# Kernel tuning notes

Hardware: AMD Instinct MI355X
Metric: run time of the kernel (lower is better)

Reference implementation:

```python
import jax, jax.numpy as jnp
import numpy as np

N_NODES = 100000
N_EDGES = 1600000
D = 128
K = 3
LEAKY_ALPHA = 0.2  # tf.nn.leaky_relu default
L2_EPS = 1e-12     # tf.math.l2_normalize default


def spmm(row, col, val, x, n_nodes):
    # y[r] = sum_{e: row[e]==r} val[e] * x[col[e]]
    return jax.ops.segment_sum(val[:, None] * x[col], row, num_segments=n_nodes)


def setup_inputs() -> dict:
    key = jax.random.key(0)
    ks = jax.random.split(key, 8)
    embeddings = jax.random.normal(ks[0], (N_NODES, D), dtype=jnp.float32) * 0.1
    edge_row = jax.random.randint(ks[1], (N_EDGES,), 0, N_NODES, dtype=jnp.int32)
    edge_col = jax.random.randint(ks[2], (N_EDGES,), 0, N_NODES, dtype=jnp.int32)
    # normalized-laplacian-like positive weights
    edge_val = jax.random.uniform(ks[3], (N_EDGES,), dtype=jnp.float32) * 0.05
    W_gc = jax.random.normal(ks[4], (K, D, D), dtype=jnp.float32) * (1.0 / np.sqrt(D))
    b_gc = jax.random.normal(ks[5], (K, D), dtype=jnp.float32) * 0.01
    W_bi = jax.random.normal(ks[6], (K, D, D), dtype=jnp.float32) * (1.0 / np.sqrt(D))
    b_bi = jax.random.normal(ks[7], (K, D), dtype=jnp.float32) * 0.01
    return {"embeddings": embeddings, "edge_row": edge_row, "edge_col": edge_col,
            "edge_val": edge_val, "W_gc": W_gc, "b_gc": b_gc, "W_bi": W_bi, "b_bi": b_bi}


def reference(embeddings, edge_row, edge_col, edge_val, W_gc, b_gc, W_bi, b_bi):
    n = embeddings.shape[0]
    x = embeddings
    depth_embeddings = [x]
    for i in range(W_gc.shape[0]):
        Lx = spmm(edge_row, edge_col, edge_val, x, n)   # L @ x  (L has zero diag)
        prop = Lx + x                                    # S @ x, S = L with diag 1
        emb = prop @ W_gc[i] + b_gc[i][None, :]
        bi = (x * Lx) @ W_bi[i] + b_bi[i][None, :]
        x = jax.nn.leaky_relu(emb + bi, negative_slope=LEAKY_ALPHA)
        sq = jnp.sum(x * x, axis=1, keepdims=True)
        norm_x = x / jnp.sqrt(jnp.maximum(sq, L2_EPS))   # tf l2_normalize semantics
        depth_embeddings.append(norm_x)
        x = norm_x  # note: original feeds normalized x to next layer via loop var? see notes
    return jnp.concatenate(depth_embeddings, axis=1)  # [N, (K+1)*D]
```

## Files before the change

kernel.cpp:

```cpp
#include <hip/hip_runtime.h>
#include <hip/hip_bf16.h>

#define ND 128
#define LDO 512
#define ALPHA 0.2f
#define L2EPS 1e-12f
#define SCAN_B 256
#define NCHUNK 256
#define RPB 512

typedef __attribute__((ext_vector_type(8))) short short8;
typedef __attribute__((ext_vector_type(4))) float f32x4;
typedef __attribute__((ext_vector_type(2))) float f32x2;

__device__ __forceinline__ short f2bf(float f) {
    union { float f; unsigned u; } c; c.f = f;
    unsigned u = c.u;
    unsigned r = (u + 0x7fffu + ((u >> 16) & 1u)) >> 16;
    return (short)r;
}
__device__ __forceinline__ float bf2f(unsigned short u) {
    union { unsigned u; float f; } c; c.u = ((unsigned)u) << 16;
    return c.f;
}
__device__ __forceinline__ void gload_lds16(const void* g, void* l) {
    __builtin_amdgcn_global_load_lds(
        (const __attribute__((address_space(1))) unsigned int*)g,
        (__attribute__((address_space(3))) unsigned int*)l, 16, 0, 0);
}

__global__ void copy_emb_kernel(const float* __restrict__ emb, float* __restrict__ out,
                                unsigned short* __restrict__ xb,
                                unsigned int* __restrict__ xf8w, int n) {
    int idx = blockIdx.x * blockDim.x + threadIdx.x;
    int total = n * 32;
    if (idx >= total) return;
    int r = idx >> 5, c4 = idx & 31;
    const float4 v = *reinterpret_cast<const float4*>(emb + (size_t)r * ND + c4 * 4);
    *reinterpret_cast<float4*>(out + (size_t)r * LDO + c4 * 4) = v;
    ushort4 b;
    b.x = (unsigned short)f2bf(v.x); b.y = (unsigned short)f2bf(v.y);
    b.z = (unsigned short)f2bf(v.z); b.w = (unsigned short)f2bf(v.w);
    *reinterpret_cast<ushort4*>(xb + (size_t)r * ND + c4 * 4) = b;
    unsigned int u = __builtin_amdgcn_cvt_pk_fp8_f32(v.x, v.y, 0, false);
    u = __builtin_amdgcn_cvt_pk_fp8_f32(v.z, v.w, u, true);
    xf8w[(size_t)r * 32 + c4] = u;
}

__global__ __launch_bounds__(256) void bucket_hist_kernel(const int* __restrict__ erow,
                                                          int* __restrict__ gcnt,
                                                          int n_edges, int nb, int ch) {
    __shared__ int cnt[256];
    int b = blockIdx.x;
    cnt[threadIdx.x] = 0;
    __syncthreads();
    int s = b * ch, e = min(n_edges, s + ch);
    for (int j = s + threadIdx.x; j < e; j += 256) {
        atomicAdd(&cnt[erow[j] >> 9], 1);
    }
    __syncthreads();
    for (int i = threadIdx.x; i < nb; i += 256) gcnt[i * NCHUNK + b] = cnt[i];
}

__global__ __launch_bounds__(SCAN_B) void scanA_kernel(const int* __restrict__ in,
                                                       int* __restrict__ outp,
                                                       int* __restrict__ partials, int n) {
    __shared__ int sm[SCAN_B];
    int i = blockIdx.x * SCAN_B + threadIdx.x;
    int v = (i < n) ? in[i] : 0;
    sm[threadIdx.x] = v;
    __syncthreads();
#pragma unroll
    for (int off = 1; off < SCAN_B; off <<= 1) {
        int t = (threadIdx.x >= off) ? sm[threadIdx.x - off] : 0;
        __syncthreads();
        sm[threadIdx.x] += t;
        __syncthreads();
    }
    if (i < n) outp[i] = sm[threadIdx.x] - v;
    if (threadIdx.x == SCAN_B - 1) partials[blockIdx.x] = sm[SCAN_B - 1];
}

__device__ __forceinline__ void scan_partials(const int* __restrict__ part, int* psc, int nb) {
    int t = threadIdx.x;
    int v = (t < nb) ? part[t] : 0;
    psc[t] = v;
    __syncthreads();
#pragma unroll
    for (int off = 1; off < 256; off <<= 1) {
        int u = (t >= off) ? psc[t - off] : 0;
        __syncthreads();
        psc[t] += u;
        __syncthreads();
    }
    int ex = psc[t] - v;
    __syncthreads();
    psc[t] = ex;
    __syncthreads();
}

__global__ __launch_bounds__(256) void bucket_scatter_kernel(const int* __restrict__ erow,
                                                             const int* __restrict__ ecol,
                                                             const float* __restrict__ eval,
                                                             const int* __restrict__ gscan,
                                                             const int* __restrict__ part,
                                                             int2* __restrict__ tmp,
                                                             int n_edges, int nb, int ch) {
    __shared__ int psc[256];
    __shared__ int cur[256];
    int b = blockIdx.x;
    scan_partials(part, psc, nb);
    for (int i = threadIdx.x; i < nb; i += 256)
        cur[i] = gscan[i * NCHUNK + b] + psc[i];
    __syncthreads();
    int s = b * ch, e = min(n_edges, s + ch);
    for (int j = s + threadIdx.x; j < e; j += 256) {
        int r = erow[j];
        int pos = atomicAdd(&cur[r >> 9], 1);
        int2 p;
        p.x = ecol[j] | ((r & (RPB - 1)) << 17);
        p.y = __float_as_int(eval[j]);
        tmp[pos] = p;
    }
}

__global__ __launch_bounds__(256) void bucket_sort_kernel(const int2* __restrict__ tmp,
                                                          const int* __restrict__ part,
                                                          int2* __restrict__ pv,
                                                          int* __restrict__ row_start,
                                                          int n, int n_edges, int nb) {
    __shared__ int psc[256];
    __shared__ int hist[RPB];
    __shared__ int cur[RPB];
    __shared__ int sc[256];
    const int t = threadIdx.x;
    const int bkt = blockIdx.x;
    const int r0 = bkt << 9;
    scan_partials(part, psc, nb);
    const int s = psc[bkt];
    const int e = (bkt + 1 < nb) ? psc[bkt + 1] : n_edges;

    for (int i = t; i < RPB; i += 256) hist[i] = 0;
    __syncthreads();
    for (int j = s + t; j < e; j += 256) atomicAdd(&hist[tmp[j].x >> 17], 1);
    __syncthreads();
    int a0 = hist[2 * t], a1 = hist[2 * t + 1];
    sc[t] = a0 + a1;
    __syncthreads();
#pragma unroll
    for (int off = 1; off < 256; off <<= 1) {
        int v = (t >= off) ? sc[t - off] : 0;
        __syncthreads();
        sc[t] += v;
        __syncthreads();
    }
    int base = s + sc[t] - a0 - a1;
    cur[2 * t] = base;
    cur[2 * t + 1] = base + a0;
    __syncthreads();
    int r1 = min(n, r0 + RPB);
    for (int i = t; i < r1 - r0; i += 256) row_start[r0 + i] = cur[i];
    if (t == 0 && r1 == n) row_start[n] = n_edges;
    __syncthreads();
    for (int j = s + t; j < e; j += 256) {
        int2 p = tmp[j];
        int pos = atomicAdd(&cur[p.x >> 17], 1);
        int2 q;
        q.x = p.x & 0x1FFFF;
        q.y = p.y;
        pv[pos] = q;
    }
}

__global__ __launch_bounds__(256) void spmm_axm_kernel(const int* __restrict__ row_start,
                                                       const int2* __restrict__ pv,
                                                       const unsigned char* __restrict__ xf8,
                                                       const unsigned short* __restrict__ xb,
                                                       unsigned short* __restrict__ Axm, int n) {
    int r = blockIdx.x * 32 + (threadIdx.x >> 3);
    if (r >= n) return;
    int l = threadIdx.x & 7;
    int s = row_start[r], e = row_start[r + 1];
    float a[16];
#pragma unroll
    for (int q = 0; q < 16; ++q) a[q] = 0.f;
    int j = s;
    for (; j + 1 < e; j += 2) {
        int2 p0 = pv[j], p1 = pv[j + 1];
        uint4 q0 = *reinterpret_cast<const uint4*>(xf8 + (size_t)p0.x * ND + l * 16);
        uint4 q1 = *reinterpret_cast<const uint4*>(xf8 + (size_t)p1.x * ND + l * 16);
        float v0 = __int_as_float(p0.y), v1 = __int_as_float(p1.y);
        f32x2 c;
        c = __builtin_amdgcn_cvt_pk_f32_fp8(q0.x, false); a[0]  += v0 * c.x; a[1]  += v0 * c.y;
        c = __builtin_amdgcn_cvt_pk_f32_fp8(q0.x, true);  a[2]  += v0 * c.x; a[3]  += v0 * c.y;
        c = __builtin_amdgcn_cvt_pk_f32_fp8(q0.y, false); a[4]  += v0 * c.x; a[5]  += v0 * c.y;
        c = __builtin_amdgcn_cvt_pk_f32_fp8(q0.y, true);  a[6]  += v0 * c.x; a[7]  += v0 * c.y;
        c = __builtin_amdgcn_cvt_pk_f32_fp8(q0.z, false); a[8]  += v0 * c.x; a[9]  += v0 * c.y;
        c = __builtin_amdgcn_cvt_pk_f32_fp8(q0.z, true);  a[10] += v0 * c.x; a[11] += v0 * c.y;
        c = __builtin_amdgcn_cvt_pk_f32_fp8(q0.w, false); a[12] += v0 * c.x; a[13] += v0 * c.y;
        c = __builtin_amdgcn_cvt_pk_f32_fp8(q0.w, true);  a[14] += v0 * c.x; a[15] += v0 * c.y;
        c = __builtin_amdgcn_cvt_pk_f32_fp8(q1.x, false); a[0]  += v1 * c.x; a[1]  += v1 * c.y;
        c = __builtin_amdgcn_cvt_pk_f32_fp8(q1.x, true);  a[2]  += v1 * c.x; a[3]  += v1 * c.y;
        c = __builtin_amdgcn_cvt_pk_f32_fp8(q1.y, false); a[4]  += v1 * c.x; a[5]  += v1 * c.y;
        c = __builtin_amdgcn_cvt_pk_f32_fp8(q1.y, true);  a[6]  += v1 * c.x; a[7]  += v1 * c.y;
        c = __builtin_amdgcn_cvt_pk_f32_fp8(q1.z, false); a[8]  += v1 * c.x; a[9]  += v1 * c.y;
        c = __builtin_amdgcn_cvt_pk_f32_fp8(q1.z, true);  a[10] += v1 * c.x; a[11] += v1 * c.y;
        c = __builtin_amdgcn_cvt_pk_f32_fp8(q1.w, false); a[12] += v1 * c.x; a[13] += v1 * c.y;
        c = __builtin_amdgcn_cvt_pk_f32_fp8(q1.w, true);  a[14] += v1 * c.x; a[15] += v1 * c.y;
    }
    if (j < e) {
        int2 p0 = pv[j];
        uint4 q0 = *reinterpret_cast<const uint4*>(xf8 + (size_t)p0.x * ND + l * 16);
        float v0 = __int_as_float(p0.y);
        f32x2 c;
        c = __builtin_amdgcn_cvt_pk_f32_fp8(q0.x, false); a[0]  += v0 * c.x; a[1]  += v0 * c.y;
        c = __builtin_amdgcn_cvt_pk_f32_fp8(q0.x, true);  a[2]  += v0 * c.x; a[3]  += v0 * c.y;
        c = __builtin_amdgcn_cvt_pk_f32_fp8(q0.y, false); a[4]  += v0 * c.x; a[5]  += v0 * c.y;
        c = __builtin_amdgcn_cvt_pk_f32_fp8(q0.y, true);  a[6]  += v0 * c.x; a[7]  += v0 * c.y;
        c = __builtin_amdgcn_cvt_pk_f32_fp8(q0.z, false); a[8]  += v0 * c.x; a[9]  += v0 * c.y;
        c = __builtin_amdgcn_cvt_pk_f32_fp8(q0.z, true);  a[10] += v0 * c.x; a[11] += v0 * c.y;
        c = __builtin_amdgcn_cvt_pk_f32_fp8(q0.w, false); a[12] += v0 * c.x; a[13] += v0 * c.y;
        c = __builtin_amdgcn_cvt_pk_f32_fp8(q0.w, true);  a[14] += v0 * c.x; a[15] += v0 * c.y;
    }
    const unsigned short* xr = xb + (size_t)r * ND + l * 16;
    short8 xv0 = *reinterpret_cast<const short8*>(xr);
    short8 xv1 = *reinterpret_cast<const short8*>(xr + 8);
    short8 pr0, pr1, xm0, xm1;
#pragma unroll
    for (int q = 0; q < 8; ++q) {
        float x0 = bf2f((unsigned short)xv0[q]);
        float x1 = bf2f((unsigned short)xv1[q]);
        pr0[q] = f2bf(x0 + a[q]);
        xm0[q] = f2bf(x0 * a[q]);
        pr1[q] = f2bf(x1 + a[8 + q]);
        xm1[q] = f2bf(x1 * a[8 + q]);
    }
    int sz = r & 7;
    int c0 = 2 * l, c1 = 2 * l + 1;
    unsigned short* rowp = Axm + (size_t)r * 256;
    *reinterpret_cast<short8*>(rowp + ((c0        ^ sz) << 3)) = pr0;
    *reinterpret_cast<short8*>(rowp + ((c1        ^ sz) << 3)) = pr1;
    *reinterpret_cast<short8*>(rowp + (((16 + c0) ^ sz) << 3)) = xm0;
    *reinterpret_cast<short8*>(rowp + (((16 + c1) ^ sz) << 3)) = xm1;
}

__global__ void prep_w_kernel(const float* __restrict__ Wgc, const float* __restrict__ bgc,
                              const float* __restrict__ Wbi, const float* __restrict__ bbi,
                              short* __restrict__ Wt2, float* __restrict__ bsum) {
    int z = blockIdx.x;
    int k = blockIdx.y;
    int t = threadIdx.x;
    int nn = t & 127;
    int h  = (t < 128) ? 0 : 1;
    const float* src = h ? (Wbi + ((size_t)z * 128 + k) * 128)
                         : (Wgc + ((size_t)z * 128 + k) * 128);
    float v = src[nn];
    int idx16 = k >> 3, e8 = k & 7;
    size_t addr = ((size_t)(z * 2 + h) * 128 + nn) * 128 + ((idx16 ^ (nn & 7)) << 3) + e8;
    Wt2[addr] = f2bf(v);
    if (k == 0 && t < 128) bsum[z * 128 + t] = bgc[z * 128 + t] + bbi[z * 128 + t];
}

__global__ __launch_bounds__(256) void fused_layer_mfma(
        const unsigned short* __restrict__ Axm,
        const short* __restrict__ Wt2,
        const float* __restrict__ bsum,
        float* __restrict__ xout,
        unsigned short* __restrict__ xbout,
        unsigned char* __restrict__ xf8out,
        int n) {
    __shared__ short A_lds[64 * 256];
    __shared__ short W_lds[128 * 128];

    const int tid  = threadIdx.x;
    const int row0 = blockIdx.x * 64;
    const int lane = tid & 63;
    const int w    = tid >> 6;
    const int lrow = lane & 15;
    const int kgrp = lane >> 4;

    {
        const char* gA = (const char*)(Axm + (size_t)row0 * 256) + w * 8192 + lane * 16;
        char*       lA = (char*)A_lds + w * 8192;
        const char* gW = (const char*)Wt2 + w * 8192 + lane * 16;
        char*       lW = (char*)W_lds + w * 8192;
#pragma unroll
        for (int it = 0; it < 8; ++it) {
            gload_lds16(gA + it * 1024, lA + it * 1024);
            gload_lds16(gW + it * 1024, lW + it * 1024);
        }
    }
    asm volatile("s_waitcnt vmcnt(0)" ::: "memory");
    __syncthreads();

    f32x4 acc[8];
#pragma unroll
    for (int nf = 0; nf < 8; ++nf) acc[nf] = (f32x4){0.f, 0.f, 0.f, 0.f};

    const int ar  = w * 16 + lrow;
    const int as_ = ar & 7;

#pragma unroll
    for (int ksl = 0; ksl < 4; ++ksl) {
        int kkl = ksl * 4 + kgrp;
        short8 af = *reinterpret_cast<const short8*>(&A_lds[ar * 256 + ((kkl ^ as_) << 3)]);
#pragma unroll
        for (int nf = 0; nf < 8; ++nf) {
            int nr = nf * 16 + lrow;
            short8 bfr = *reinterpret_cast<const short8*>(&W_lds[nr * 128 + ((kkl ^ (nr & 7)) << 3)]);
            acc[nf] = __builtin_amdgcn_mfma_f32_16x16x32_bf16(af, bfr, acc[nf], 0, 0, 0);
        }
    }
    __syncthreads();
    {
        const char* gW = (const char*)Wt2 + 32768 + w * 8192 + lane * 16;
        char*       lW = (char*)W_lds + w * 8192;
#pragma unroll
        for (int it = 0; it < 8; ++it) gload_lds16(gW + it * 1024, lW + it * 1024);
    }
    asm volatile("s_waitcnt vmcnt(0)" ::: "memory");
    __syncthreads();

#pragma unroll
    for (int ksl = 0; ksl < 4; ++ksl) {
        int kkl = ksl * 4 + kgrp;
        short8 af = *reinterpret_cast<const short8*>(&A_lds[ar * 256 + (((16 + kkl) ^ as_) << 3)]);
#pragma unroll
        for (int nf = 0; nf < 8; ++nf) {
            int nr = nf * 16 + lrow;
            short8 bfr = *reinterpret_cast<const short8*>(&W_lds[nr * 128 + ((kkl ^ (nr & 7)) << 3)]);
            acc[nf] = __builtin_amdgcn_mfma_f32_16x16x32_bf16(af, bfr, acc[nf], 0, 0, 0);
        }
    }

    float bsv[8];
#pragma unroll
    for (int nf = 0; nf < 8; ++nf) bsv[nf] = bsum[nf * 16 + lrow];

#pragma unroll
    for (int reg = 0; reg < 4; ++reg) {
        int grow = row0 + w * 16 + kgrp * 4 + reg;
        float v[8];
        float ssq = 0.f;
#pragma unroll
        for (int nf = 0; nf < 8; ++nf) {
            float tv = acc[nf][reg] + bsv[nf];
            tv = tv > 0.f ? tv : ALPHA * tv;
            v[nf] = tv;
            ssq += tv * tv;
        }
        ssq += __shfl_xor(ssq, 1);
        ssq += __shfl_xor(ssq, 2);
        ssq += __shfl_xor(ssq, 4);
        ssq += __shfl_xor(ssq, 8);
        float sc = 1.0f / sqrtf(fmaxf(ssq, L2EPS));
        if (grow < n) {
            float* op = xout + (size_t)grow * LDO;
            unsigned short* bp = xbout + (size_t)grow * ND;
            unsigned char* fp = xf8out + (size_t)grow * ND;
#pragma unroll
            for (int nf = 0; nf < 8; ++nf) {
                float ov = v[nf] * sc;
                __builtin_nontemporal_store(ov, op + nf * 16 + lrow);
                bp[nf * 16 + lrow] = (unsigned short)f2bf(ov);
                unsigned int u8 = __builtin_amdgcn_cvt_pk_fp8_f32(ov, ov, 0, false);
                fp[nf * 16 + lrow] = (unsigned char)(u8 & 0xff);
            }
        }
    }
}

extern "C" void kernel_launch(void* const* d_in, const int* in_sizes, int n_in,
                              void* d_out, int out_size, void* d_ws, size_t ws_size,
                              hipStream_t stream) {
    const float* emb  = (const float*)d_in[0];
    const int*   erow = (const int*)d_in[1];
    const int*   ecol = (const int*)d_in[2];
    const float* eval = (const float*)d_in[3];
    const float* Wgc  = (const float*)d_in[4];
    const float* bgc  = (const float*)d_in[5];
    const float* Wbi  = (const float*)d_in[6];
    const float* bbi  = (const float*)d_in[7];
    float* out = (float*)d_out;

    const int n        = in_sizes[0] / ND;
    const int n_edges  = in_sizes[1];
    const int n_layers = in_sizes[5] / ND;

    const int nb = (n + RPB - 1) >> 9;
    const int ch = (n_edges + NCHUNK - 1) / NCHUNK;
    const int ng = nb * NCHUNK;

    char* ws = (char*)d_ws;
    size_t off = 0;
    auto alloc = [&](size_t bytes) { void* p = ws + off; off = (off + bytes + 255) & ~(size_t)255; return p; };
    unsigned short* xb  = (unsigned short*)alloc((size_t)n * ND * sizeof(short));
    unsigned char*  xf8 = (unsigned char*) alloc((size_t)n * ND);
    unsigned short* Axm = (unsigned short*)alloc((size_t)(n + 64) * 256 * sizeof(short));
    int2*  pv        = (int2*) alloc((size_t)n_edges * sizeof(int2));
    int2*  tmp       = (int2*) alloc((size_t)n_edges * sizeof(int2));
    int*   row_start = (int*)  alloc((size_t)(n + 1) * sizeof(int));
    int*   gcnt      = (int*)  alloc((size_t)ng * sizeof(int));
    int*   gscan     = (int*)  alloc((size_t)ng * sizeof(int));
    int*   partials  = (int*)  alloc(512 * sizeof(int));
    short* Wt2       = (short*)alloc((size_t)n_layers * 2 * 128 * 128 * sizeof(short));
    float* bsum      = (float*)alloc((size_t)n_layers * 128 * sizeof(float));
    (void)ws_size;

    {
        int total = n * 32;
        copy_emb_kernel<<<(total + 255) / 256, 256, 0, stream>>>(emb, out, xb,
                                                                 (unsigned int*)xf8, n);
    }

    {
        dim3 g(n_layers, 128);
        prep_w_kernel<<<g, 256, 0, stream>>>(Wgc, bgc, Wbi, bbi, Wt2, bsum);
    }

    bucket_hist_kernel<<<NCHUNK, 256, 0, stream>>>(erow, gcnt, n_edges, nb, ch);
    {
        int nblk = (ng + SCAN_B - 1) / SCAN_B;
        scanA_kernel<<<nblk, SCAN_B, 0, stream>>>(gcnt, gscan, partials, ng);
    }
    bucket_scatter_kernel<<<NCHUNK, 256, 0, stream>>>(erow, ecol, eval, gscan, partials,
                                                      tmp, n_edges, nb, ch);
    bucket_sort_kernel<<<nb, 256, 0, stream>>>(tmp, partials, pv, row_start,
                                               n, n_edges, nb);

    for (int i = 0; i < n_layers; ++i) {
        spmm_axm_kernel<<<(n + 31) / 32, 256, 0, stream>>>(row_start, pv, xf8, xb, Axm, n);
        fused_layer_mfma<<<(n + 63) / 64, 256, 0, stream>>>(
            Axm, Wt2 + (size_t)i * 2 * 128 * 128, bsum + (size_t)i * 128,
            out + (size_t)(i + 1) * ND, xb, xf8, n);
    }
}
```

Baseline: 317.4 us.

## Merge prologue kernels into one launch and prefetch second weight half into registers

Result: faster. 301.1 us (-5.2%).

```diff
diff --git a/kernel.cpp b/kernel.cpp
--- a/kernel.cpp
+++ b/kernel.cpp
@@ -29,37 +29,60 @@
         (__attribute__((address_space(3))) unsigned int*)l, 16, 0, 0);
 }
 
-__global__ void copy_emb_kernel(const float* __restrict__ emb, float* __restrict__ out,
-                                unsigned short* __restrict__ xb,
-                                unsigned int* __restrict__ xf8w, int n) {
-    int idx = blockIdx.x * blockDim.x + threadIdx.x;
-    int total = n * 32;
-    if (idx >= total) return;
-    int r = idx >> 5, c4 = idx & 31;
-    const float4 v = *reinterpret_cast<const float4*>(emb + (size_t)r * ND + c4 * 4);
-    *reinterpret_cast<float4*>(out + (size_t)r * LDO + c4 * 4) = v;
-    ushort4 b;
-    b.x = (unsigned short)f2bf(v.x); b.y = (unsigned short)f2bf(v.y);
-    b.z = (unsigned short)f2bf(v.z); b.w = (unsigned short)f2bf(v.w);
-    *reinterpret_cast<ushort4*>(xb + (size_t)r * ND + c4 * 4) = b;
-    unsigned int u = __builtin_amdgcn_cvt_pk_fp8_f32(v.x, v.y, 0, false);
-    u = __builtin_amdgcn_cvt_pk_fp8_f32(v.z, v.w, u, true);
-    xf8w[(size_t)r * 32 + c4] = u;
-}
-
-__global__ __launch_bounds__(256) void bucket_hist_kernel(const int* __restrict__ erow,
-                                                          int* __restrict__ gcnt,
-                                                          int n_edges, int nb, int ch) {
+__global__ __launch_bounds__(256) void prologue_kernel(
+        const float* __restrict__ emb, float* __restrict__ out,
+        unsigned short* __restrict__ xb, unsigned int* __restrict__ xf8w,
+        const int* __restrict__ erow, int* __restrict__ gcnt,
+        const float* __restrict__ Wgc, const float* __restrict__ bgc,
+        const float* __restrict__ Wbi, const float* __restrict__ bbi,
+        short* __restrict__ Wt2, float* __restrict__ bsum,
+        int n, int n_edges, int nb, int ch, int n_prep) {
     __shared__ int cnt[256];
-    int b = blockIdx.x;
-    cnt[threadIdx.x] = 0;
-    __syncthreads();
-    int s = b * ch, e = min(n_edges, s + ch);
-    for (int j = s + threadIdx.x; j < e; j += 256) {
-        atomicAdd(&cnt[erow[j] >> 9], 1);
-    }
-    __syncthreads();
-    for (int i = threadIdx.x; i < nb; i += 256) gcnt[i * NCHUNK + b] = cnt[i];
+    const int b = blockIdx.x;
+    const int t = threadIdx.x;
+    if (b < NCHUNK) {
+        cnt[t] = 0;
+        __syncthreads();
+        int s = b * ch, e = min(n_edges, s + ch);
+        for (int j = s + t; j < e; j += 256) atomicAdd(&cnt[erow[j] >> 9], 1);
+        __syncthreads();
+        for (int i = t; i < nb; i += 256) gcnt[i * NCHUNK + b] = cnt[i];
+    } else if (b < NCHUNK + n_prep) {
+        int zb = b - NCHUNK;
+        int z = zb >> 7, k = zb & 127;
+        int nn = t & 127;
+        int h  = (t < 128) ? 0 : 1;
+        const float* src = h ? (Wbi + ((size_t)z * 128 + k) * 128)
+                             : (Wgc + ((size_t)z * 128 + k) * 128);
+        float v = src[nn];
+        int idx16 = k >> 3, e8 = k & 7;
+        size_t addr = ((size_t)(z * 2 + h) * 128 + nn) * 128 + ((idx16 ^ (nn & 7)) << 3) + e8;
+        Wt2[addr] = f2bf(v);
+        if (k == 0 && t < 128) bsum[z * 128 + t] = bgc[z * 128 + t] + bbi[z * 128 + t];
+    } else {
+        int idx = (b - NCHUNK - n_prep) * 256 + t;
+        int total = n * 32;
+        if (idx >= total) return;
+        int r = idx >> 5, c4 = idx & 31;
+        const float* ep = emb + (size_t)r * ND + c4 * 4;
+        float4 v;
+        v.x = __builtin_nontemporal_load(ep + 0);
+        v.y = __builtin_nontemporal_load(ep + 1);
+        v.z = __builtin_nontemporal_load(ep + 2);
+        v.w = __builtin_nontemporal_load(ep + 3);
+        float* op = out + (size_t)r * LDO + c4 * 4;
+        __builtin_nontemporal_store(v.x, op + 0);
+        __builtin_nontemporal_store(v.y, op + 1);
+        __builtin_nontemporal_store(v.z, op + 2);
+        __builtin_nontemporal_store(v.w, op + 3);
+        ushort4 bb;
+        bb.x = (unsigned short)f2bf(v.x); bb.y = (unsigned short)f2bf(v.y);
+        bb.z = (unsigned short)f2bf(v.z); bb.w = (unsigned short)f2bf(v.w);
+        *reinterpret_cast<ushort4*>(xb + (size_t)r * ND + c4 * 4) = bb;
+        unsigned int u = __builtin_amdgcn_cvt_pk_fp8_f32(v.x, v.y, 0, false);
+        u = __builtin_amdgcn_cvt_pk_fp8_f32(v.z, v.w, u, true);
+        xf8w[(size_t)r * 32 + c4] = u;
+    }
 }
 
 __global__ __launch_bounds__(SCAN_B) void scanA_kernel(const int* __restrict__ in,
@@ -244,23 +267,6 @@
     *reinterpret_cast<short8*>(rowp + (((16 + c1) ^ sz) << 3)) = xm1;
 }
 
-__global__ void prep_w_kernel(const float* __restrict__ Wgc, const float* __restrict__ bgc,
-                              const float* __restrict__ Wbi, const float* __restrict__ bbi,
-                              short* __restrict__ Wt2, float* __restrict__ bsum) {
-    int z = blockIdx.x;
-    int k = blockIdx.y;
-    int t = threadIdx.x;
-    int nn = t & 127;
-    int h  = (t < 128) ? 0 : 1;
-    const float* src = h ? (Wbi + ((size_t)z * 128 + k) * 128)
-                         : (Wgc + ((size_t)z * 128 + k) * 128);
-    float v = src[nn];
-    int idx16 = k >> 3, e8 = k & 7;
-    size_t addr = ((size_t)(z * 2 + h) * 128 + nn) * 128 + ((idx16 ^ (nn & 7)) << 3) + e8;
-    Wt2[addr] = f2bf(v);
-    if (k == 0 && t < 128) bsum[z * 128 + t] = bgc[z * 128 + t] + bbi[z * 128 + t];
-}
-
 __global__ __launch_bounds__(256) void fused_layer_mfma(
         const unsigned short* __restrict__ Axm,
         const short* __restrict__ Wt2,
@@ -293,6 +299,14 @@
     asm volatile("s_waitcnt vmcnt(0)" ::: "memory");
     __syncthreads();
 
+    short8 w1r[8];
+    {
+        const char* gW1 = (const char*)Wt2 + 32768 + w * 8192 + lane * 16;
+#pragma unroll
+        for (int it = 0; it < 8; ++it)
+            w1r[it] = *reinterpret_cast<const short8*>(gW1 + it * 1024);
+    }
+
     f32x4 acc[8];
 #pragma unroll
     for (int nf = 0; nf < 8; ++nf) acc[nf] = (f32x4){0.f, 0.f, 0.f, 0.f};
@@ -313,12 +327,11 @@
     }
     __syncthreads();
     {
-        const char* gW = (const char*)Wt2 + 32768 + w * 8192 + lane * 16;
-        char*       lW = (char*)W_lds + w * 8192;
-#pragma unroll
-        for (int it = 0; it < 8; ++it) gload_lds16(gW + it * 1024, lW + it * 1024);
-    }
-    asm volatile("s_waitcnt vmcnt(0)" ::: "memory");
+        char* lW = (char*)W_lds + w * 8192 + lane * 16;
+#pragma unroll
+        for (int it = 0; it < 8; ++it)
+            *reinterpret_cast<short8*>(lW + it * 1024) = w1r[it];
+    }
     __syncthreads();
 
 #pragma unroll
@@ -408,17 +421,14 @@
     (void)ws_size;
 
     {
-        int total = n * 32;
-        copy_emb_kernel<<<(total + 255) / 256, 256, 0, stream>>>(emb, out, xb,
-                                                                 (unsigned int*)xf8, n);
-    }
-
-    {
-        dim3 g(n_layers, 128);
-        prep_w_kernel<<<g, 256, 0, stream>>>(Wgc, bgc, Wbi, bbi, Wt2, bsum);
-    }
-
-    bucket_hist_kernel<<<NCHUNK, 256, 0, stream>>>(erow, gcnt, n_edges, nb, ch);
+        int n_prep = n_layers * 128;
+        int n_copy = (n * 32 + 255) / 256;
+        int grid = NCHUNK + n_prep + n_copy;
+        prologue_kernel<<<grid, 256, 0, stream>>>(emb, out, xb, (unsigned int*)xf8,
+                                                  erow, gcnt, Wgc, bgc, Wbi, bbi,
+                                                  Wt2, bsum, n, n_edges, nb, ch, n_prep);
+    }
+
     {
         int nblk = (ng + SCAN_B - 1) / SCAN_B;
         scanA_kernel<<<nblk, SCAN_B, 0, stream>>>(gcnt, gscan, partials, ng);
```
